# Kernel optimization log

Measured on AMD Instinct MI355X. Metric: run time of the kernel, lower is better.

## Reference

```python
import jax, jax.numpy as jnp
import numpy as np

BETA = 15.0  # soft-max temperature used by the common Erosion2d/Dilation2d (soft_max=True)
EPS = 1e-5


def _morph(x, w, dilation, kind):
    """Channel-wise soft morphological op over a KxK dilated window ('same' padding).
    erosion: -logsumexp(beta*(w - patch))/beta ; dilation: logsumexp(beta*(w + patch))/beta.
    """
    B, C, H, W = x.shape
    K = w.shape[-1]
    eff = K + (K - 1) * (dilation - 1)
    pb = (eff - 1) // 2
    pe = (eff - 1) - pb
    xp = jnp.pad(x, ((0, 0), (0, 0), (pb, pe), (pb, pe)))
    taps = [xp[:, :, i * dilation:i * dilation + H, j * dilation:j * dilation + W]
            for i in range(K) for j in range(K)]
    patches = jnp.stack(taps, axis=2)                      # (B, C, K*K, H, W)
    wf = w.reshape(C, K * K, 1, 1)                          # broadcast over B, H, W
    z = (wf - patches) if kind == 'erosion' else (wf + patches)
    out = jax.scipy.special.logsumexp(z * BETA, axis=2) / BETA  # (B, C, H, W)
    return -out if kind == 'erosion' else out


def _bn(x, gamma, beta):
    """BatchNorm2d in training mode: batch statistics over (B, H, W) per channel."""
    mean = jnp.mean(x, axis=(0, 2, 3), keepdims=True)
    var = jnp.var(x, axis=(0, 2, 3), keepdims=True)
    g = gamma.reshape(1, -1, 1, 1)
    b = beta.reshape(1, -1, 1, 1)
    return g * (x - mean) * jax.lax.rsqrt(var + EPS) + b


def setup_inputs() -> dict:
    key = jax.random.key(0)
    ks = jax.random.split(key, 5)
    B, C, H, W, K = 8, 64, 192, 192, 3
    x = jax.random.normal(ks[0], (B, C, H, W), jnp.float32)
    # morphology structuring elements (torch init is zeros; small randn for a nontrivial test)
    we = jax.random.normal(ks[1], (3, C, K, K), jnp.float32) * 0.1
    wd = jax.random.normal(ks[2], (3, C, K, K), jnp.float32) * 0.1
    # per-branch BN affine params (torch default: gamma=1, beta=0)
    bn_ge = jnp.ones((3, C), jnp.float32)
    bn_be = jnp.zeros((3, C), jnp.float32)
    bn_gd = jnp.ones((3, C), jnp.float32)
    bn_bd = jnp.zeros((3, C), jnp.float32)
    # 1x1 conv (3C -> 1, no bias): weight (1, 3C, 1, 1) stored flat as (3C,)
    conve_w = jax.random.normal(ks[3], (3 * C,), jnp.float32) * 0.05
    convd_w = jax.random.normal(ks[4], (3 * C,), jnp.float32) * 0.05
    g_e = jnp.ones((1,), jnp.float32)
    b_e = jnp.zeros((1,), jnp.float32)
    g_d = jnp.ones((1,), jnp.float32)
    b_d = jnp.zeros((1,), jnp.float32)
    return dict(x=x, we=we, wd=wd, bn_ge=bn_ge, bn_be=bn_be, bn_gd=bn_gd, bn_bd=bn_bd,
                conve_w=conve_w, convd_w=convd_w, g_e=g_e, b_e=b_e, g_d=g_d, b_d=b_d)


def reference(x, we, wd, bn_ge, bn_be, bn_gd, bn_bd, conve_w, convd_w, g_e, b_e, g_d, b_d):
    # three erosion branches (dilations 1,2,3), each followed by its own BN
    xe = jnp.concatenate([
        _bn(_morph(x, we[i], i + 1, 'erosion'), bn_ge[i], bn_be[i]) for i in range(3)
    ], axis=1)                                              # (B, 3C, H, W)
    xd = jnp.concatenate([
        _bn(_morph(x, wd[i], i + 1, 'dilation'), bn_gd[i], bn_bd[i]) for i in range(3)
    ], axis=1)
    # 1x1 conv to 1 channel + BN + ReLU
    ye = jnp.einsum('bchw,c->bhw', xe, conve_w)[:, None]    # (B, 1, H, W)
    ye = jax.nn.relu(_bn(ye, g_e, b_e))
    yd = jnp.einsum('bchw,c->bhw', xd, convd_w)[:, None]
    yd = jax.nn.relu(_bn(yd, g_d, b_d))
    return jnp.concatenate([ye, yd], axis=1)                # (B, 2, H, W)
```

## Files before the change

### kernel.cpp

```cpp
#include <hip/hip_runtime.h>


#define BETA 15.0f
#define MSHIFT 25.0f
#define INV_BETA (1.0f/15.0f)
#define LN2 0.6931471805599453f
#define EPSB 1e-5f
#define Hn 192
#define Wn 192
#define HWn (192*192)
#define N1 (8*192*192)
#define SFLOOR 1e-37f

#define STDH 70
#define STW 38
#define STSTR 39
#define STNL (STDH*STW)

#define RDH 38
#define RSTR 39
#define RNL (RDH*STW)
#define RNITER 6

#define WS_SUM   0
#define WS_SQS   384
#define WS_SCAL  768
#define WS_WG    772
#define WS_YE    (772 + 3456)
#define WS_YD    (WS_YE + 294912)
#define WS_SLAB  (WS_YE + 2*294912)

__global__ void k_wexp(const float* __restrict__ we,
                       const float* __restrict__ wd,
                       float* __restrict__ wg) {
    int idx = blockIdx.x * 256 + threadIdx.x;
    if (idx >= 3456) return;
    int kb = idx / 576;
    int rem = idx - kb * 576;
    float w = (kb < 3) ? we[kb * 576 + rem] : wd[(kb - 3) * 576 + rem];
    wg[idx] = __expf(BETA * w);
}

template<int D, int H, int STR>
__device__ __forceinline__ void sweepT(const float* __restrict__ P,
                                       int py0, int px,
                                       const float* __restrict__ wgp,
                                       float* __restrict__ S) {
    float W[9];
#pragma unroll
    for (int k2 = 0; k2 < 9; ++k2) W[k2] = wgp[k2];
#pragma unroll
    for (int k = 0; k < H; ++k) S[k] = 0.f;
    const float* base = P + (py0 - D + 3) * STR + (px - D);
#pragma unroll
    for (int r = 0; r < H + 2 * D; ++r) {
        float va = base[r * STR];
        float vb = base[r * STR + D];
        float vc = base[r * STR + 2 * D];
#pragma unroll
        for (int i = 0; i < 3; ++i) {
            int k = r - i * D;
            if (k >= 0 && k < H) {
                S[k] = fmaf(W[i*3+0], va, S[k]);
                S[k] = fmaf(W[i*3+1], vb, S[k]);
                S[k] = fmaf(W[i*3+2], vc, S[k]);
            }
        }
    }
}

__device__ __forceinline__ void red2(float a, float b2, int lane, float* rs, float* rq) {
#pragma unroll
    for (int off = 32; off; off >>= 1) {
        a  += __shfl_down(a, off, 64);
        b2 += __shfl_down(b2, off, 64);
    }
    if (lane == 0) { *rs = a; *rq = b2; }
}

__global__ __launch_bounds__(256, 7) void k_stats(
    const float* __restrict__ x, const float* __restrict__ wg,
    float* __restrict__ sum, float* __restrict__ sqs) {
    __shared__ float EX[STDH * STSTR], EY[STDH * STSTR];
    __shared__ float redS[4][6], redQ[4][6];
    const int tid = threadIdx.x;
    const int p = blockIdx.y;
    const int c = p & 63;
    const int t = blockIdx.x;
    const int h0 = (t / 6) * 64, w0 = (t % 6) * 32;

    const float* xp = x + (size_t)p * HWn;
    {
        int r = tid / STW, cc = tid - r * STW;
        for (int l = tid; l < STNL; l += 256) {
            int gh = h0 - 3 + r, gw = w0 - 3 + cc;
            float v = 0.f;
            if ((unsigned)gh < (unsigned)Hn && (unsigned)gw < (unsigned)Wn)
                v = xp[gh * Wn + gw];
            float bx = BETA * v;
            EX[r * STSTR + cc] = __expf(-bx - MSHIFT);
            EY[r * STSTR + cc] = __expf( bx - MSHIFT);
            r += 6; cc += 28;
            if (cc >= STW) { cc -= STW; ++r; }
        }
    }
    __syncthreads();

    const int px = (tid & 31) + 3;
    const int py0 = (tid >> 5) * 8;
    const int lane = tid & 63, wv = tid >> 6;
    const float LI = LN2 * INV_BETA, MI = MSHIFT * INV_BETA;

#define DO_BR_STATS(D, SLOT, PL, AL, AM) { \
    float S[8]; \
    sweepT<D, 8, STSTR>(PL, py0, px, wg + (SLOT) * 576 + c * 9, S); \
    float sv = 0.f, qv = 0.f; \
    _Pragma("unroll") \
    for (int k = 0; k < 8; ++k) { \
        float m = fmaf(__log2f(fmaxf(S[k], SFLOOR)), AL, AM); \
        sv += m; qv = fmaf(m, m, qv); \
    } \
    red2(sv, qv, lane, &redS[wv][SLOT], &redQ[wv][SLOT]); }

    DO_BR_STATS(1, 0, EX, -LI, -MI)
    DO_BR_STATS(2, 1, EX, -LI, -MI)
    DO_BR_STATS(3, 2, EX, -LI, -MI)
    DO_BR_STATS(1, 3, EY,  LI,  MI)
    DO_BR_STATS(2, 4, EY,  LI,  MI)
    DO_BR_STATS(3, 5, EY,  LI,  MI)

    __syncthreads();
    if (tid < 6)
        atomicAdd(&sum[tid * 64 + c],
                  redS[0][tid] + redS[1][tid] + redS[2][tid] + redS[3][tid]);
    else if (tid < 12) {
        int v = tid - 6;
        atomicAdd(&sqs[v * 64 + c],
                  redQ[0][v] + redQ[1][v] + redQ[2][v] + redQ[3][v]);
    }
}

template<int NS>
__global__ __launch_bounds__(256, 4) void k_reduce(
    const float* __restrict__ x, const float* __restrict__ wg,
    const float* __restrict__ sum, const float* __restrict__ sqs,
    const float* __restrict__ bn_ge, const float* __restrict__ bn_gd,
    const float* __restrict__ conve, const float* __restrict__ convd,
    float* __restrict__ ye, float* __restrict__ yd,
    float* __restrict__ slab, float* __restrict__ scal) {
    constexpr int NC = 64 / NS;
    __shared__ float EX[RDH * RSTR], EY[RDH * RSTR];
    __shared__ float al[384];
    __shared__ float redA[4][4];
    const int tid = threadIdx.x;
    const int t = blockIdx.x;
    const int b = blockIdx.y;
    const int grp = blockIdx.z;
    const int c0 = grp * NC;
    const int tr = t / 6, tc = t - tr * 6;
    const int h0 = tr * 32, w0 = tc * 32;
    const int px = (tid & 31) + 3;
    const int py0 = (tid >> 5) * 4;
    const float* xb = x + (size_t)b * 64 * HWn;

    for (int l = tid; l < 384; l += 256) {
        int side_ = l / 192, ch = l - side_ * 192;
        float mean = sum[l] * (1.0f / N1);
        float var  = sqs[l] * (1.0f / N1) - mean * mean;
        float inv  = rsqrtf(fmaxf(var, 0.f) + EPSB);
        float g  = side_ ? bn_gd[ch] : bn_ge[ch];
        float cw = side_ ? convd[ch] : conve[ch];
        float sgn = side_ ? 1.f : -1.f;
        al[l] = sgn * cw * g * inv * INV_BETA * LN2;
    }

    float accE[4] = {0.f, 0.f, 0.f, 0.f}, accD[4] = {0.f, 0.f, 0.f, 0.f};
    float L[RNITER];

    {
        const float* xp = xb + (size_t)c0 * HWn;
        int r = tid / STW, cc = tid - r * STW;
#pragma unroll
        for (int i = 0; i < RNITER; ++i) {
            int l = tid + i * 256;
            float v = 0.f;
            if (l < RNL) {
                int gh = h0 - 3 + r, gw = w0 - 3 + cc;
                if ((unsigned)gh < (unsigned)Hn && (unsigned)gw < (unsigned)Wn)
                    v = xp[gh * Wn + gw];
            }
            L[i] = v;
            r += 6; cc += 28;
            if (cc >= STW) { cc -= STW; ++r; }
        }
    }

    for (int ci = 0; ci < NC; ++ci) {
        __syncthreads();
        {
            int r = tid / STW, cc = tid - r * STW;
#pragma unroll
            for (int i = 0; i < RNITER; ++i) {
                int l = tid + i * 256;
                if (l < RNL) {
                    float bx = BETA * L[i];
                    EX[r * RSTR + cc] = __expf(-bx - MSHIFT);
                    EY[r * RSTR + cc] = __expf( bx - MSHIFT);
                }
                r += 6; cc += 28;
                if (cc >= STW) { cc -= STW; ++r; }
            }
        }
        __syncthreads();
        if (ci < NC - 1) {
            const float* xp = xb + (size_t)(c0 + ci + 1) * HWn;
            int r = tid / STW, cc = tid - r * STW;
#pragma unroll
            for (int i = 0; i < RNITER; ++i) {
                int l = tid + i * 256;
                float v = 0.f;
                if (l < RNL) {
                    int gh = h0 - 3 + r, gw = w0 - 3 + cc;
                    if ((unsigned)gh < (unsigned)Hn && (unsigned)gw < (unsigned)Wn)
                        v = xp[gh * Wn + gw];
                }
                L[i] = v;
                r += 6; cc += 28;
                if (cc >= STW) { cc -= STW; ++r; }
            }
        }
        const int c = c0 + ci;
#define DO_BR_ACC(D, SIDE, BR, PL, ACC) { \
        float S[4]; \
        sweepT<D, 4, RSTR>(PL, py0, px, wg + ((SIDE) * 3 + (BR)) * 576 + c * 9, S); \
        const float a_ = al[(SIDE) * 192 + (BR) * 64 + c]; \
        _Pragma("unroll") \
        for (int k = 0; k < 4; ++k) \
            ACC[k] = fmaf(a_, __log2f(fmaxf(S[k], SFLOOR)), ACC[k]); }

        DO_BR_ACC(1, 0, 0, EX, accE)
        DO_BR_ACC(2, 0, 1, EX, accE)
        DO_BR_ACC(3, 0, 2, EX, accE)
        DO_BR_ACC(1, 1, 0, EY, accD)
        DO_BR_ACC(2, 1, 1, EY, accD)
        DO_BR_ACC(3, 1, 2, EY, accD)
    }

    if constexpr (NS == 1) {
        const int oidx = b * HWn + (h0 + py0) * Wn + (w0 + px - 3);
#pragma unroll
        for (int k = 0; k < 4; ++k) {
            ye[oidx + k * Wn] = accE[k];
            yd[oidx + k * Wn] = accD[k];
        }
        float se = 0.f, qe = 0.f, sd = 0.f, qd = 0.f;
#pragma unroll
        for (int k = 0; k < 4; ++k) {
            se += accE[k]; qe = fmaf(accE[k], accE[k], qe);
            sd += accD[k]; qd = fmaf(accD[k], accD[k], qd);
        }
        const int lane = tid & 63, wv = tid >> 6;
        float v4[4] = {se, qe, sd, qd};
#pragma unroll
        for (int j = 0; j < 4; ++j) {
            float tv = v4[j];
#pragma unroll
            for (int off = 32; off; off >>= 1) tv += __shfl_down(tv, off, 64);
            if (lane == 0) redA[wv][j] = tv;
        }
        __syncthreads();
        if (tid < 4)
            atomicAdd(&scal[tid],
                      redA[0][tid] + redA[1][tid] + redA[2][tid] + redA[3][tid]);
    } else {
        float* pe = slab + ((size_t)grp * 8 + b) * HWn;
        float* pd = slab + ((size_t)(NS + grp) * 8 + b) * HWn;
        const int oidx = (h0 + py0) * Wn + (w0 + px - 3);
#pragma unroll
        for (int k = 0; k < 4; ++k) {
            pe[oidx + k * Wn] = accE[k];
            pd[oidx + k * Wn] = accD[k];
        }
    }
}

template<int NS>
__global__ __launch_bounds__(256) void k_fsum(
    const float* __restrict__ slab,
    float* __restrict__ ye, float* __restrict__ yd, float* __restrict__ scal) {
    int i = blockIdx.x * 256 + threadIdx.x;
    int b = i / HWn, rem = i - b * HWn;
    float e = 0.f, d = 0.f;
#pragma unroll
    for (int g = 0; g < NS; ++g) {
        e += slab[((size_t)g * 8 + b) * HWn + rem];
        d += slab[((size_t)(NS + g) * 8 + b) * HWn + rem];
    }
    ye[i] = e; yd[i] = d;
    float v[4] = {e, e * e, d, d * d};
    __shared__ float red[4][4];
    int lane = threadIdx.x & 63, wv = threadIdx.x >> 6;
#pragma unroll
    for (int k = 0; k < 4; ++k) {
        float tv = v[k];
#pragma unroll
        for (int off = 32; off; off >>= 1) tv += __shfl_down(tv, off, 64);
        if (lane == 0) red[wv][k] = tv;
    }
    __syncthreads();
    if (threadIdx.x < 4)
        atomicAdd(&scal[threadIdx.x],
                  red[0][threadIdx.x] + red[1][threadIdx.x] + red[2][threadIdx.x] + red[3][threadIdx.x]);
}

__global__ __launch_bounds__(256) void k_final(
    const float* __restrict__ ye, const float* __restrict__ yd,
    const float* __restrict__ scal,
    const float* __restrict__ g_e, const float* __restrict__ b_e,
    const float* __restrict__ g_d, const float* __restrict__ b_d,
    float* __restrict__ out) {
    int i = blockIdx.x * 256 + threadIdx.x;
    float me_ = scal[0] * (1.0f / N1);
    float ve  = scal[1] * (1.0f / N1) - me_ * me_;
    float ie  = rsqrtf(fmaxf(ve, 0.f) + EPSB);
    float md_ = scal[2] * (1.0f / N1);
    float vd  = scal[3] * (1.0f / N1) - md_ * md_;
    float idv = rsqrtf(fmaxf(vd, 0.f) + EPSB);
    float ge = g_e[0], be = b_e[0];
    float gd = g_d[0], bd = b_d[0];
    int b = i / HWn, rem = i - b * HWn;
    float oe = fmaxf(ge * (ye[i] - me_) * ie + be, 0.f);
    float od = fmaxf(gd * (yd[i] - md_) * idv + bd, 0.f);
    out[(size_t)(b * 2) * HWn + rem]     = oe;
    out[(size_t)(b * 2 + 1) * HWn + rem] = od;
}

extern "C" void kernel_launch(void* const* d_in, const int* in_sizes, int n_in,
                              void* d_out, int out_size, void* d_ws, size_t ws_size,
                              hipStream_t stream) {
    const float* x     = (const float*)d_in[0];
    const float* we    = (const float*)d_in[1];
    const float* wd    = (const float*)d_in[2];
    const float* bn_ge = (const float*)d_in[3];
    const float* bn_gd = (const float*)d_in[5];
    const float* conve = (const float*)d_in[7];
    const float* convd = (const float*)d_in[8];
    const float* g_e   = (const float*)d_in[9];
    const float* b_e   = (const float*)d_in[10];
    const float* g_d   = (const float*)d_in[11];
    const float* b_d   = (const float*)d_in[12];
    float* ws = (float*)d_ws;

    const size_t need4 = (size_t)(WS_SLAB + 4 * 2 * 294912) * sizeof(float);
    const size_t need2 = (size_t)(WS_SLAB + 2 * 2 * 294912) * sizeof(float);
    const int ns = (ws_size >= need4) ? 4 : (ws_size >= need2) ? 2 : 1;

    hipMemsetAsync(d_ws, 0, 772 * sizeof(float), stream);
    hipLaunchKernelGGL(k_wexp, dim3(14), dim3(256), 0, stream, we, wd, ws + WS_WG);
    hipLaunchKernelGGL(k_stats, dim3(18, 512), dim3(256), 0, stream,
                       x, ws + WS_WG, ws + WS_SUM, ws + WS_SQS);
    if (ns == 4) {
        hipLaunchKernelGGL((k_reduce<4>), dim3(36, 8, 4), dim3(256), 0, stream,
                           x, ws + WS_WG, ws + WS_SUM, ws + WS_SQS, bn_ge, bn_gd,
                           conve, convd, ws + WS_YE, ws + WS_YD, ws + WS_SLAB,
                           ws + WS_SCAL);
        hipLaunchKernelGGL((k_fsum<4>), dim3(1152), dim3(256), 0, stream,
                           ws + WS_SLAB, ws + WS_YE, ws + WS_YD, ws + WS_SCAL);
    } else if (ns == 2) {
        hipLaunchKernelGGL((k_reduce<2>), dim3(36, 8, 2), dim3(256), 0, stream,
                           x, ws + WS_WG, ws + WS_SUM, ws + WS_SQS, bn_ge, bn_gd,
                           conve, convd, ws + WS_YE, ws + WS_YD, ws + WS_SLAB,
                           ws + WS_SCAL);
        hipLaunchKernelGGL((k_fsum<2>), dim3(1152), dim3(256), 0, stream,
                           ws + WS_SLAB, ws + WS_YE, ws + WS_YD, ws + WS_SCAL);
    } else {
        hipLaunchKernelGGL((k_reduce<1>), dim3(36, 8, 1), dim3(256), 0, stream,
                           x, ws + WS_WG, ws + WS_SUM, ws + WS_SQS, bn_ge, bn_gd,
                           conve, convd, ws + WS_YE, ws + WS_YD, ws, ws + WS_SCAL);
    }
    hipLaunchKernelGGL(k_final, dim3(1152), dim3(256), 0, stream,
                       ws + WS_YE, ws + WS_YD, ws + WS_SCAL, g_e, b_e, g_d, b_d,
                       (float*)d_out);
}
```

Measured before the change: 280.2 us.

## Fuse all stages into one cooperative persistent kernel with grid syncs

Replaces the memset, weight-exp, stats, reduce, fsum and finalize launches with a single cooperative kernel of 1152 blocks. It separates the phases with grid.sync(), and the stats phase loops over its 9216 work units. The aim is to remove launch gaps and the tail effects between kernels. In exchange, stats now runs under a launch bound of 5 blocks per CU instead of 7, the shared buffers are sized for the larger stats tile, and there are four grid-wide barriers. If cooperative launch or the occupancy check fails, it falls back to the old multi-kernel path.

Result: no change. 280.7 us (+0.2%).

```diff
diff --git a/kernel.cpp b/kernel.cpp
--- a/kernel.cpp
+++ b/kernel.cpp
@@ -1,4 +1,7 @@
 #include <hip/hip_runtime.h>
+#include <hip/hip_cooperative_groups.h>
+
+namespace cg = cooperative_groups;
 
 
 #define BETA 15.0f
@@ -29,17 +32,7 @@
 #define WS_YE    (772 + 3456)
 #define WS_YD    (WS_YE + 294912)
 #define WS_SLAB  (WS_YE + 2*294912)
-
-__global__ void k_wexp(const float* __restrict__ we,
-                       const float* __restrict__ wd,
-                       float* __restrict__ wg) {
-    int idx = blockIdx.x * 256 + threadIdx.x;
-    if (idx >= 3456) return;
-    int kb = idx / 576;
-    int rem = idx - kb * 576;
-    float w = (kb < 3) ? we[kb * 576 + rem] : wd[(kb - 3) * 576 + rem];
-    wg[idx] = __expf(BETA * w);
-}
+#define NBLK 1152
 
 template<int D, int H, int STR>
 __device__ __forceinline__ void sweepT(const float* __restrict__ P,
@@ -78,17 +71,14 @@
     if (lane == 0) { *rs = a; *rq = b2; }
 }
 
-__global__ __launch_bounds__(256, 7) void k_stats(
+__device__ __forceinline__ void stats_unit(
     const float* __restrict__ x, const float* __restrict__ wg,
-    float* __restrict__ sum, float* __restrict__ sqs) {
-    __shared__ float EX[STDH * STSTR], EY[STDH * STSTR];
-    __shared__ float redS[4][6], redQ[4][6];
-    const int tid = threadIdx.x;
-    const int p = blockIdx.y;
+    float* __restrict__ sum, float* __restrict__ sqs,
+    int t, int p, int tid,
+    float* __restrict__ EX, float* __restrict__ EY,
+    float (*redS)[6], float (*redQ)[6]) {
     const int c = p & 63;
-    const int t = blockIdx.x;
     const int h0 = (t / 6) * 64, w0 = (t % 6) * 32;
-
     const float* xp = x + (size_t)p * HWn;
     {
         int r = tid / STW, cc = tid - r * STW;
@@ -128,6 +118,7 @@
     DO_BR_STATS(1, 3, EY,  LI,  MI)
     DO_BR_STATS(2, 4, EY,  LI,  MI)
     DO_BR_STATS(3, 5, EY,  LI,  MI)
+#undef DO_BR_STATS
 
     __syncthreads();
     if (tid < 6)
@@ -140,29 +131,11 @@
     }
 }
 
-template<int NS>
-__global__ __launch_bounds__(256, 4) void k_reduce(
-    const float* __restrict__ x, const float* __restrict__ wg,
+__device__ __forceinline__ void alpha_fill(
     const float* __restrict__ sum, const float* __restrict__ sqs,
     const float* __restrict__ bn_ge, const float* __restrict__ bn_gd,
     const float* __restrict__ conve, const float* __restrict__ convd,
-    float* __restrict__ ye, float* __restrict__ yd,
-    float* __restrict__ slab, float* __restrict__ scal) {
-    constexpr int NC = 64 / NS;
-    __shared__ float EX[RDH * RSTR], EY[RDH * RSTR];
-    __shared__ float al[384];
-    __shared__ float redA[4][4];
-    const int tid = threadIdx.x;
-    const int t = blockIdx.x;
-    const int b = blockIdx.y;
-    const int grp = blockIdx.z;
-    const int c0 = grp * NC;
-    const int tr = t / 6, tc = t - tr * 6;
-    const int h0 = tr * 32, w0 = tc * 32;
-    const int px = (tid & 31) + 3;
-    const int py0 = (tid >> 5) * 4;
-    const float* xb = x + (size_t)b * 64 * HWn;
-
+    float* __restrict__ al, int tid) {
     for (int l = tid; l < 384; l += 256) {
         int side_ = l / 192, ch = l - side_ * 192;
         float mean = sum[l] * (1.0f / N1);
@@ -173,6 +146,24 @@
         float sgn = side_ ? 1.f : -1.f;
         al[l] = sgn * cw * g * inv * INV_BETA * LN2;
     }
+}
+
+template<int NS>
+__device__ __forceinline__ void reduce_unit(
+    const float* __restrict__ x, const float* __restrict__ wg,
+    const float* __restrict__ al,
+    float* __restrict__ ye, float* __restrict__ yd,
+    float* __restrict__ slab, float* __restrict__ scal,
+    int t, int b, int grp, int tid,
+    float* __restrict__ EX, float* __restrict__ EY,
+    float (*redA)[4]) {
+    constexpr int NC = 64 / NS;
+    const int c0 = grp * NC;
+    const int tr = t / 6, tc = t - tr * 6;
+    const int h0 = tr * 32, w0 = tc * 32;
+    const int px = (tid & 31) + 3;
+    const int py0 = (tid >> 5) * 4;
+    const float* xb = x + (size_t)b * 64 * HWn;
 
     float accE[4] = {0.f, 0.f, 0.f, 0.f}, accD[4] = {0.f, 0.f, 0.f, 0.f};
     float L[RNITER];
@@ -244,6 +235,7 @@
         DO_BR_ACC(1, 1, 0, EY, accD)
         DO_BR_ACC(2, 1, 1, EY, accD)
         DO_BR_ACC(3, 1, 2, EY, accD)
+#undef DO_BR_ACC
     }
 
     if constexpr (NS == 1) {
@@ -282,6 +274,118 @@
             pd[oidx + k * Wn] = accD[k];
         }
     }
+}
+
+__global__ __launch_bounds__(256, 5) void k_fused(
+    const float* __restrict__ x,
+    const float* __restrict__ we, const float* __restrict__ wd,
+    const float* __restrict__ bn_ge, const float* __restrict__ bn_gd,
+    const float* __restrict__ conve, const float* __restrict__ convd,
+    const float* __restrict__ g_e, const float* __restrict__ b_e,
+    const float* __restrict__ g_d, const float* __restrict__ b_d,
+    float* __restrict__ out,
+    float* __restrict__ wg, float* __restrict__ sum, float* __restrict__ sqs,
+    float* __restrict__ scal, float* __restrict__ slab) {
+    __shared__ float EX[STDH * STSTR], EY[STDH * STSTR];
+    __shared__ float redS[4][6], redQ[4][6];
+    __shared__ float al[384];
+    __shared__ float redA[4][4];
+    cg::grid_group grid = cg::this_grid();
+    const int tid = threadIdx.x;
+    const int bid = blockIdx.x;
+    const int gidx = bid * 256 + tid;
+
+    if (gidx < 772) sum[gidx] = 0.f;
+    if (gidx < 3456) {
+        int kb = gidx / 576, rem = gidx - kb * 576;
+        float w = (kb < 3) ? we[kb * 576 + rem] : wd[(kb - 3) * 576 + rem];
+        wg[gidx] = __expf(BETA * w);
+    }
+    grid.sync();
+
+    for (int u = bid; u < 9216; u += NBLK)
+        stats_unit(x, wg, sum, sqs, u % 18, u / 18, tid, EX, EY, redS, redQ);
+    grid.sync();
+
+    alpha_fill(sum, sqs, bn_ge, bn_gd, conve, convd, al, tid);
+    {
+        int t = bid % 36, b = (bid / 36) & 7, grp = bid / 288;
+        reduce_unit<4>(x, wg, al, nullptr, nullptr, slab, scal,
+                       t, b, grp, tid, EX, EY, redA);
+    }
+    grid.sync();
+
+    const int i = gidx;
+    const int b = i / HWn, rem = i - b * HWn;
+    float e = 0.f, d = 0.f;
+#pragma unroll
+    for (int g = 0; g < 4; ++g) {
+        e += slab[((size_t)g * 8 + b) * HWn + rem];
+        d += slab[((size_t)(4 + g) * 8 + b) * HWn + rem];
+    }
+    {
+        float v4[4] = {e, e * e, d, d * d};
+        const int lane = tid & 63, wv = tid >> 6;
+#pragma unroll
+        for (int k = 0; k < 4; ++k) {
+            float tv = v4[k];
+#pragma unroll
+            for (int off = 32; off; off >>= 1) tv += __shfl_down(tv, off, 64);
+            if (lane == 0) redA[wv][k] = tv;
+        }
+        __syncthreads();
+        if (tid < 4)
+            atomicAdd(&scal[tid],
+                      redA[0][tid] + redA[1][tid] + redA[2][tid] + redA[3][tid]);
+    }
+    grid.sync();
+
+    float me_ = scal[0] * (1.0f / N1);
+    float ve  = scal[1] * (1.0f / N1) - me_ * me_;
+    float ie  = rsqrtf(fmaxf(ve, 0.f) + EPSB);
+    float md_ = scal[2] * (1.0f / N1);
+    float vd  = scal[3] * (1.0f / N1) - md_ * md_;
+    float idv = rsqrtf(fmaxf(vd, 0.f) + EPSB);
+    float oe = fmaxf(g_e[0] * (e - me_) * ie + b_e[0], 0.f);
+    float od = fmaxf(g_d[0] * (d - md_) * idv + b_d[0], 0.f);
+    out[(size_t)(b * 2) * HWn + rem]     = oe;
+    out[(size_t)(b * 2 + 1) * HWn + rem] = od;
+}
+
+__global__ void k_wexp(const float* __restrict__ we,
+                       const float* __restrict__ wd,
+                       float* __restrict__ wg) {
+    int idx = blockIdx.x * 256 + threadIdx.x;
+    if (idx >= 3456) return;
+    int kb = idx / 576;
+    int rem = idx - kb * 576;
+    float w = (kb < 3) ? we[kb * 576 + rem] : wd[(kb - 3) * 576 + rem];
+    wg[idx] = __expf(BETA * w);
+}
+
+__global__ __launch_bounds__(256, 7) void k_stats(
+    const float* __restrict__ x, const float* __restrict__ wg,
+    float* __restrict__ sum, float* __restrict__ sqs) {
+    __shared__ float EX[STDH * STSTR], EY[STDH * STSTR];
+    __shared__ float redS[4][6], redQ[4][6];
+    stats_unit(x, wg, sum, sqs, blockIdx.x, blockIdx.y, threadIdx.x,
+               EX, EY, redS, redQ);
+}
+
+template<int NS>
+__global__ __launch_bounds__(256, 4) void k_reduce(
+    const float* __restrict__ x, const float* __restrict__ wg,
+    const float* __restrict__ sum, const float* __restrict__ sqs,
+    const float* __restrict__ bn_ge, const float* __restrict__ bn_gd,
+    const float* __restrict__ conve, const float* __restrict__ convd,
+    float* __restrict__ ye, float* __restrict__ yd,
+    float* __restrict__ slab, float* __restrict__ scal) {
+    __shared__ float EX[RDH * RSTR], EY[RDH * RSTR];
+    __shared__ float al[384];
+    __shared__ float redA[4][4];
+    alpha_fill(sum, sqs, bn_ge, bn_gd, conve, convd, al, threadIdx.x);
+    reduce_unit<NS>(x, wg, al, ye, yd, slab, scal,
+                    blockIdx.x, blockIdx.y, blockIdx.z, threadIdx.x, EX, EY, redA);
 }
 
 template<int NS>
@@ -350,6 +454,37 @@
     const float* g_d   = (const float*)d_in[11];
     const float* b_d   = (const float*)d_in[12];
     float* ws = (float*)d_ws;
+    float* outp = (float*)d_out;
+
+    const size_t needC = (size_t)(WS_SLAB + 8 * 294912) * sizeof(float);
+
+    static int coop = -1;
+    if (coop < 0) {
+        int dev = 0; hipGetDevice(&dev);
+        int cl = 0;
+        hipDeviceGetAttribute(&cl, hipDeviceAttributeCooperativeLaunch, dev);
+        int ncu = 0;
+        hipDeviceGetAttribute(&ncu, hipDeviceAttributeMultiprocessorCount, dev);
+        int maxb = 0;
+        hipOccupancyMaxActiveBlocksPerMultiprocessor(&maxb, (const void*)k_fused, 256, 0);
+        coop = (cl && (long)maxb * ncu >= NBLK) ? 1 : 0;
+    }
+
+    if (coop == 1 && ws_size >= needC) {
+        float* wg   = ws + WS_WG;
+        float* sum  = ws + WS_SUM;
+        float* sqs  = ws + WS_SQS;
+        float* scal = ws + WS_SCAL;
+        float* slab = ws + WS_SLAB;
+        void* kargs[] = {
+            (void*)&x, (void*)&we, (void*)&wd, (void*)&bn_ge, (void*)&bn_gd,
+            (void*)&conve, (void*)&convd, (void*)&g_e, (void*)&b_e,
+            (void*)&g_d, (void*)&b_d, (void*)&outp,
+            (void*)&wg, (void*)&sum, (void*)&sqs, (void*)&scal, (void*)&slab };
+        hipLaunchCooperativeKernel((const void*)k_fused, dim3(NBLK), dim3(256),
+                                   kargs, 0, stream);
+        return;
+    }
 
     const size_t need4 = (size_t)(WS_SLAB + 4 * 2 * 294912) * sizeof(float);
     const size_t need2 = (size_t)(WS_SLAB + 2 * 2 * 294912) * sizeof(float);
```

## Widen stats tiles to 64x64 with two-column-per-thread sweeps and paired loads

Applied to the files above, without the earlier changes.

The stats kernel now covers 64x64 tiles, so the grid is halved. Each thread computes two adjacent output columns through a new sweep2 routine that reads float2 values from shared memory and reuses taps between the two columns. Halo staging in both kernels now loads pairs of elements and writes float2 to shared memory, with strides padded to 72 and 40. The memset is folded into the weight-exp kernel to save a launch. The costs are more registers per thread (launch bounds drop to 3 blocks per SM) and possible shared-memory bank conflicts from the new stride.

New measurement: 282.0 us. About the same (+0.7%).

```diff
diff --git a/kernel.cpp b/kernel.cpp
--- a/kernel.cpp
+++ b/kernel.cpp
@@ -13,14 +13,14 @@
 #define SFLOOR 1e-37f
 
 #define STDH 70
-#define STW 38
-#define STSTR 39
-#define STNL (STDH*STW)
+#define STDW 70
+#define STSTR 72
+#define SNPAIR (STDH*35)
 
 #define RDH 38
-#define RSTR 39
-#define RNL (RDH*STW)
-#define RNITER 6
+#define RSTR 40
+#define RNPAIR (RDH*19)
+#define RPITER 3
 
 #define WS_SUM   0
 #define WS_SQS   384
@@ -32,13 +32,14 @@
 
 __global__ void k_wexp(const float* __restrict__ we,
                        const float* __restrict__ wd,
-                       float* __restrict__ wg) {
+                       float* __restrict__ ws) {
     int idx = blockIdx.x * 256 + threadIdx.x;
+    if (idx < 772) ws[idx] = 0.f;
     if (idx >= 3456) return;
     int kb = idx / 576;
     int rem = idx - kb * 576;
     float w = (kb < 3) ? we[kb * 576 + rem] : wd[(kb - 3) * 576 + rem];
-    wg[idx] = __expf(BETA * w);
+    ws[WS_WG + idx] = __expf(BETA * w);
 }
 
 template<int D, int H, int STR>
@@ -69,6 +70,52 @@
     }
 }
 
+template<int D>
+__device__ __forceinline__ void sweep2(const float* __restrict__ P,
+                                       int py0, int tcol,
+                                       const float* __restrict__ wgp,
+                                       float* __restrict__ SA,
+                                       float* __restrict__ SB) {
+    float W[9];
+#pragma unroll
+    for (int k2 = 0; k2 < 9; ++k2) W[k2] = wgp[k2];
+#pragma unroll
+    for (int k = 0; k < 8; ++k) { SA[k] = 0.f; SB[k] = 0.f; }
+    const int colbase = (D == 1) ? (2 * tcol + 2) : (2 * tcol);
+#pragma unroll
+    for (int r = 0; r < 8 + 2 * D; ++r) {
+        const float2* row =
+            (const float2*)(P + (py0 - D + 3 + r) * STSTR + colbase);
+        float2 v0 = row[0], v1 = row[1];
+        float ta0, ta1, ta2, tb0, tb1, tb2;
+        if (D == 1) {
+            ta0 = v0.x; ta1 = v0.y; ta2 = v1.x;
+            tb0 = v0.y; tb1 = v1.x; tb2 = v1.y;
+        } else {
+            float2 v2 = row[2], v3 = row[3];
+            if (D == 2) {
+                ta0 = v0.y; ta1 = v1.y; ta2 = v2.y;
+                tb0 = v1.x; tb1 = v2.x; tb2 = v3.x;
+            } else {
+                ta0 = v0.x; ta1 = v1.y; ta2 = v3.x;
+                tb0 = v0.y; tb1 = v2.x; tb2 = v3.y;
+            }
+        }
+#pragma unroll
+        for (int i = 0; i < 3; ++i) {
+            int k = r - i * D;
+            if (k >= 0 && k < 8) {
+                SA[k] = fmaf(W[i*3+0], ta0, SA[k]);
+                SA[k] = fmaf(W[i*3+1], ta1, SA[k]);
+                SA[k] = fmaf(W[i*3+2], ta2, SA[k]);
+                SB[k] = fmaf(W[i*3+0], tb0, SB[k]);
+                SB[k] = fmaf(W[i*3+1], tb1, SB[k]);
+                SB[k] = fmaf(W[i*3+2], tb2, SB[k]);
+            }
+        }
+    }
+}
+
 __device__ __forceinline__ void red2(float a, float b2, int lane, float* rs, float* rq) {
 #pragma unroll
     for (int off = 32; off; off >>= 1) {
@@ -78,7 +125,7 @@
     if (lane == 0) { *rs = a; *rq = b2; }
 }
 
-__global__ __launch_bounds__(256, 7) void k_stats(
+__global__ __launch_bounds__(256, 3) void k_stats(
     const float* __restrict__ x, const float* __restrict__ wg,
     float* __restrict__ sum, float* __restrict__ sqs) {
     __shared__ float EX[STDH * STSTR], EY[STDH * STSTR];
@@ -87,38 +134,44 @@
     const int p = blockIdx.y;
     const int c = p & 63;
     const int t = blockIdx.x;
-    const int h0 = (t / 6) * 64, w0 = (t % 6) * 32;
+    const int h0 = (t / 3) * 64, w0 = (t % 3) * 64;
 
     const float* xp = x + (size_t)p * HWn;
     {
-        int r = tid / STW, cc = tid - r * STW;
-        for (int l = tid; l < STNL; l += 256) {
-            int gh = h0 - 3 + r, gw = w0 - 3 + cc;
-            float v = 0.f;
-            if ((unsigned)gh < (unsigned)Hn && (unsigned)gw < (unsigned)Wn)
-                v = xp[gh * Wn + gw];
-            float bx = BETA * v;
-            EX[r * STSTR + cc] = __expf(-bx - MSHIFT);
-            EY[r * STSTR + cc] = __expf( bx - MSHIFT);
-            r += 6; cc += 28;
-            if (cc >= STW) { cc -= STW; ++r; }
+        int r = tid / 35, pp = tid - r * 35;
+        for (int l = tid; l < SNPAIR; l += 256) {
+            int gh = h0 - 3 + r;
+            int gw0 = w0 - 3 + 2 * pp;
+            float va = 0.f, vb = 0.f;
+            if ((unsigned)gh < (unsigned)Hn) {
+                if ((unsigned)gw0 < (unsigned)Wn)       va = xp[gh * Wn + gw0];
+                if ((unsigned)(gw0+1) < (unsigned)Wn)   vb = xp[gh * Wn + gw0 + 1];
+            }
+            float ba = BETA * va, bb = BETA * vb;
+            *(float2*)&EX[r * STSTR + 2 * pp] =
+                make_float2(__expf(-ba - MSHIFT), __expf(-bb - MSHIFT));
+            *(float2*)&EY[r * STSTR + 2 * pp] =
+                make_float2(__expf( ba - MSHIFT), __expf( bb - MSHIFT));
+            r += 7; pp += 11;
+            if (pp >= 35) { pp -= 35; ++r; }
         }
     }
     __syncthreads();
 
-    const int px = (tid & 31) + 3;
+    const int tcol = tid & 31;
     const int py0 = (tid >> 5) * 8;
     const int lane = tid & 63, wv = tid >> 6;
     const float LI = LN2 * INV_BETA, MI = MSHIFT * INV_BETA;
 
 #define DO_BR_STATS(D, SLOT, PL, AL, AM) { \
-    float S[8]; \
-    sweepT<D, 8, STSTR>(PL, py0, px, wg + (SLOT) * 576 + c * 9, S); \
+    float SA[8], SB[8]; \
+    sweep2<D>(PL, py0, tcol, wg + (SLOT) * 576 + c * 9, SA, SB); \
     float sv = 0.f, qv = 0.f; \
     _Pragma("unroll") \
     for (int k = 0; k < 8; ++k) { \
-        float m = fmaf(__log2f(fmaxf(S[k], SFLOOR)), AL, AM); \
-        sv += m; qv = fmaf(m, m, qv); \
+        float ma = fmaf(__log2f(fmaxf(SA[k], SFLOOR)), AL, AM); \
+        float mb = fmaf(__log2f(fmaxf(SB[k], SFLOOR)), AL, AM); \
+        sv += ma + mb; qv = fmaf(ma, ma, fmaf(mb, mb, qv)); \
     } \
     red2(sv, qv, lane, &redS[wv][SLOT], &redQ[wv][SLOT]); }
 
@@ -128,6 +181,7 @@
     DO_BR_STATS(1, 3, EY,  LI,  MI)
     DO_BR_STATS(2, 4, EY,  LI,  MI)
     DO_BR_STATS(3, 5, EY,  LI,  MI)
+#undef DO_BR_STATS
 
     __syncthreads();
     if (tid < 6)
@@ -137,6 +191,23 @@
         int v = tid - 6;
         atomicAdd(&sqs[v * 64 + c],
                   redQ[0][v] + redQ[1][v] + redQ[2][v] + redQ[3][v]);
+    }
+}
+
+__device__ __forceinline__ void alpha_fill(
+    const float* __restrict__ sum, const float* __restrict__ sqs,
+    const float* __restrict__ bn_ge, const float* __restrict__ bn_gd,
+    const float* __restrict__ conve, const float* __restrict__ convd,
+    float* __restrict__ al, int tid) {
+    for (int l = tid; l < 384; l += 256) {
+        int side_ = l / 192, ch = l - side_ * 192;
+        float mean = sum[l] * (1.0f / N1);
+        float var  = sqs[l] * (1.0f / N1) - mean * mean;
+        float inv  = rsqrtf(fmaxf(var, 0.f) + EPSB);
+        float g  = side_ ? bn_gd[ch] : bn_ge[ch];
+        float cw = side_ ? convd[ch] : conve[ch];
+        float sgn = side_ ? 1.f : -1.f;
+        al[l] = sgn * cw * g * inv * INV_BETA * LN2;
     }
 }
 
@@ -163,70 +234,67 @@
     const int py0 = (tid >> 5) * 4;
     const float* xb = x + (size_t)b * 64 * HWn;
 
-    for (int l = tid; l < 384; l += 256) {
-        int side_ = l / 192, ch = l - side_ * 192;
-        float mean = sum[l] * (1.0f / N1);
-        float var  = sqs[l] * (1.0f / N1) - mean * mean;
-        float inv  = rsqrtf(fmaxf(var, 0.f) + EPSB);
-        float g  = side_ ? bn_gd[ch] : bn_ge[ch];
-        float cw = side_ ? convd[ch] : conve[ch];
-        float sgn = side_ ? 1.f : -1.f;
-        al[l] = sgn * cw * g * inv * INV_BETA * LN2;
-    }
+    alpha_fill(sum, sqs, bn_ge, bn_gd, conve, convd, al, tid);
 
     float accE[4] = {0.f, 0.f, 0.f, 0.f}, accD[4] = {0.f, 0.f, 0.f, 0.f};
-    float L[RNITER];
+    float2 L[RPITER];
 
     {
         const float* xp = xb + (size_t)c0 * HWn;
-        int r = tid / STW, cc = tid - r * STW;
-#pragma unroll
-        for (int i = 0; i < RNITER; ++i) {
+        int r = tid / 19, pp = tid - r * 19;
+#pragma unroll
+        for (int i = 0; i < RPITER; ++i) {
             int l = tid + i * 256;
-            float v = 0.f;
-            if (l < RNL) {
-                int gh = h0 - 3 + r, gw = w0 - 3 + cc;
-                if ((unsigned)gh < (unsigned)Hn && (unsigned)gw < (unsigned)Wn)
-                    v = xp[gh * Wn + gw];
-            }
-            L[i] = v;
-            r += 6; cc += 28;
-            if (cc >= STW) { cc -= STW; ++r; }
+            float va = 0.f, vb = 0.f;
+            if (l < RNPAIR) {
+                int gh = h0 - 3 + r, gw0 = w0 - 3 + 2 * pp;
+                if ((unsigned)gh < (unsigned)Hn) {
+                    if ((unsigned)gw0 < (unsigned)Wn)     va = xp[gh * Wn + gw0];
+                    if ((unsigned)(gw0+1) < (unsigned)Wn) vb = xp[gh * Wn + gw0 + 1];
+                }
+            }
+            L[i] = make_float2(va, vb);
+            r += 13; pp += 9;
+            if (pp >= 19) { pp -= 19; ++r; }
         }
     }
 
     for (int ci = 0; ci < NC; ++ci) {
         __syncthreads();
         {
-            int r = tid / STW, cc = tid - r * STW;
-#pragma unroll
-            for (int i = 0; i < RNITER; ++i) {
+            int r = tid / 19, pp = tid - r * 19;
+#pragma unroll
+            for (int i = 0; i < RPITER; ++i) {
                 int l = tid + i * 256;
-                if (l < RNL) {
-                    float bx = BETA * L[i];
-                    EX[r * RSTR + cc] = __expf(-bx - MSHIFT);
-                    EY[r * RSTR + cc] = __expf( bx - MSHIFT);
+                if (l < RNPAIR) {
+                    float ba = BETA * L[i].x, bb = BETA * L[i].y;
+                    *(float2*)&EX[r * RSTR + 2 * pp] =
+                        make_float2(__expf(-ba - MSHIFT), __expf(-bb - MSHIFT));
+                    *(float2*)&EY[r * RSTR + 2 * pp] =
+                        make_float2(__expf( ba - MSHIFT), __expf( bb - MSHIFT));
                 }
-                r += 6; cc += 28;
-                if (cc >= STW) { cc -= STW; ++r; }
+                r += 13; pp += 9;
+                if (pp >= 19) { pp -= 19; ++r; }
             }
         }
         __syncthreads();
         if (ci < NC - 1) {
             const float* xp = xb + (size_t)(c0 + ci + 1) * HWn;
-            int r = tid / STW, cc = tid - r * STW;
-#pragma unroll
-            for (int i = 0; i < RNITER; ++i) {
+            int r = tid / 19, pp = tid - r * 19;
+#pragma unroll
+            for (int i = 0; i < RPITER; ++i) {
                 int l = tid + i * 256;
-                float v = 0.f;
-                if (l < RNL) {
-                    int gh = h0 - 3 + r, gw = w0 - 3 + cc;
-                    if ((unsigned)gh < (unsigned)Hn && (unsigned)gw < (unsigned)Wn)
-                        v = xp[gh * Wn + gw];
+                float va = 0.f, vb = 0.f;
+                if (l < RNPAIR) {
+                    int gh = h0 - 3 + r, gw0 = w0 - 3 + 2 * pp;
+                    if ((unsigned)gh < (unsigned)Hn) {
+                        if ((unsigned)gw0 < (unsigned)Wn)     va = xp[gh * Wn + gw0];
+                        if ((unsigned)(gw0+1) < (unsigned)Wn) vb = xp[gh * Wn + gw0 + 1];
+                    }
                 }
-                L[i] = v;
-                r += 6; cc += 28;
-                if (cc >= STW) { cc -= STW; ++r; }
+                L[i] = make_float2(va, vb);
+                r += 13; pp += 9;
+                if (pp >= 19) { pp -= 19; ++r; }
             }
         }
         const int c = c0 + ci;
@@ -244,6 +312,7 @@
         DO_BR_ACC(1, 1, 0, EY, accD)
         DO_BR_ACC(2, 1, 1, EY, accD)
         DO_BR_ACC(3, 1, 2, EY, accD)
+#undef DO_BR_ACC
     }
 
     if constexpr (NS == 1) {
@@ -355,9 +424,8 @@
     const size_t need2 = (size_t)(WS_SLAB + 2 * 2 * 294912) * sizeof(float);
     const int ns = (ws_size >= need4) ? 4 : (ws_size >= need2) ? 2 : 1;
 
-    hipMemsetAsync(d_ws, 0, 772 * sizeof(float), stream);
-    hipLaunchKernelGGL(k_wexp, dim3(14), dim3(256), 0, stream, we, wd, ws + WS_WG);
-    hipLaunchKernelGGL(k_stats, dim3(18, 512), dim3(256), 0, stream,
+    hipLaunchKernelGGL(k_wexp, dim3(14), dim3(256), 0, stream, we, wd, ws);
+    hipLaunchKernelGGL(k_stats, dim3(9, 512), dim3(256), 0, stream,
                        x, ws + WS_WG, ws + WS_SUM, ws + WS_SQS);
     if (ns == 4) {
         hipLaunchKernelGGL((k_reduce<4>), dim3(36, 8, 4), dim3(256), 0, stream,
```
